# Optimization experiments

Hardware: AMD Instinct MI355X
Metric: run time of the kernel (lower is better)

The kernel has to match this reference:

```python
import jax, jax.numpy as jnp
import numpy as np

EPS = 1e-6
TTT_BASE_LR = 1.0
NUM_HEADS = 16


def _ln_fused_l2_bwd(x, l2_target, gamma, beta, eps=EPS):
    # Gradient of ||LN(x)*gamma+beta - target||^2/2 wrt x (fused LN + L2 bwd).
    mu = x.mean(axis=-1, keepdims=True)
    var = ((x - mu) ** 2).mean(axis=-1, keepdims=True)
    std = jnp.sqrt(var + eps)
    x_hat = (x - mu) / std
    grad_x_hat = (gamma * x_hat + beta - l2_target) * gamma
    z = (grad_x_hat
         - grad_x_hat.mean(axis=-1, keepdims=True)
         - x_hat * (grad_x_hat * x_hat).mean(axis=-1, keepdims=True)) / std
    return z


def _ln_fwd(x, gamma, beta, eps=EPS):
    mu = x.mean(axis=-1, keepdims=True)
    var = ((x - mu) ** 2).mean(axis=-1, keepdims=True)
    x_hat = (x - mu) / jnp.sqrt(var + eps)
    return gamma * x_hat + beta


def setup_inputs() -> dict:
    key = jax.random.key(0)
    ks = jax.random.split(key, 6)
    B, L, C, H = 2, 2048, 1024, NUM_HEADS
    D = C // H
    return {
        "hidden_states": jax.random.normal(ks[0], (B, L, C), jnp.float32),
        "Wq": jax.random.normal(ks[1], (C, C), jnp.float32) * 0.02,
        "Wk": jax.random.normal(ks[2], (C, C), jnp.float32) * 0.02,
        "Wv": jax.random.normal(ks[3], (C, C), jnp.float32) * 0.02,
        "W1": jax.random.normal(ks[4], (H, D, D), jnp.float32) * 0.02,
        "b1": jnp.zeros((H, 1, D), jnp.float32),
        "ttt_norm_weight": jnp.ones((H, D), jnp.float32),
        "ttt_norm_bias": jnp.zeros((H, D), jnp.float32),
        "lr_weight": jax.random.normal(ks[5], (H, C, 1), jnp.float32) * 0.02,
        "lr_bias": jnp.zeros((H, 1), jnp.float32),
    }


def reference(hidden_states, Wq, Wk, Wv, W1, b1,
              ttt_norm_weight, ttt_norm_bias, lr_weight, lr_bias):
    B, L, C = hidden_states.shape
    H = NUM_HEADS
    D = C // H

    def proj(W):  # nn.Linear(no bias): x @ W^T, then split heads -> [B,H,L,D]
        return (hidden_states @ W.T).reshape(B, L, H, D).transpose(0, 2, 1, 3)

    XQ, XK, XV = proj(Wq), proj(Wk), proj(Wv)

    # adaptive per-token learning rate eta: [B,H,L,1]
    ttt_lr = jnp.einsum("blc,hci->bhli", hidden_states, lr_weight)
    ttt_lr = jax.nn.sigmoid(ttt_lr + lr_bias.reshape(1, H, 1, 1))
    eta = TTT_BASE_LR * ttt_lr / D

    # inner-loop forward with initial fast weights W1,b1
    Z1 = jnp.einsum("bhld,hdf->bhlf", XK, W1) + b1[None]  # [B,H,L,D]
    recon_target = XV - XK

    gamma = ttt_norm_weight.reshape(1, H, 1, D)
    beta = ttt_norm_bias.reshape(1, H, 1, D)
    grad_l_wrt_Z1 = _ln_fused_l2_bwd(Z1, recon_target, gamma, beta)

    # dual form update (batch-parallel, no state carry)
    eg = eta * grad_l_wrt_Z1                               # [B,H,L,D]
    Attn1 = jnp.einsum("bhld,bhmd->bhlm", XQ, XK)          # [B,H,L,L]
    b1_bar = b1[None] - eg.sum(axis=2, keepdims=True)      # [B,H,1,D]
    Z1_bar = (jnp.einsum("bhld,hdf->bhlf", XQ, W1)
              - jnp.einsum("bhlm,bhmd->bhld", Attn1, eg)
              + b1_bar)

    Z1_normalized = _ln_fwd(Z1_bar, gamma, beta)
    return XQ + Z1_normalized  # [B,H,L,D]
```

## Files before the change

kernel.cpp:

```cpp
#include <hip/hip_runtime.h>
#include <math.h>

#define B_ 2
#define L_ 2048
#define C_ 1024
#define H_ 16
#define D_ 64
#define BH_ (B_*H_)
#define M_ (B_*L_)
#define N_ (3*C_)
#define K_ C_
#define EPS_ 1e-6f
#define NCHUNK_ 16
#define LDT_ 136
#define WTS_ 72

typedef unsigned short ushort_t;
typedef short short8 __attribute__((ext_vector_type(8)));
typedef float f32x4 __attribute__((ext_vector_type(4)));
typedef unsigned short ushort4_t __attribute__((ext_vector_type(4)));

__device__ __forceinline__ ushort_t f2bf(float f) {
    union { float f; unsigned u; } v; v.f = f;
    unsigned r = v.u + 0x7FFFu + ((v.u >> 16) & 1u);
    return (ushort_t)(r >> 16);
}
__device__ __forceinline__ float bf2f(ushort_t h) {
    union { unsigned u; float f; } v; v.u = ((unsigned)h) << 16;
    return v.f;
}

__device__ __forceinline__ void gload16(const void* g, void* l) {
    __builtin_amdgcn_global_load_lds(
        (const __attribute__((address_space(1))) void*)g,
        (__attribute__((address_space(3))) void*)l, 16, 0, 0);
}

__global__ __launch_bounds__(256) void cast_eta(
    const float* __restrict__ hs, const float* __restrict__ Wq,
    const float* __restrict__ Wk, const float* __restrict__ Wv,
    const float* __restrict__ W1, const float* __restrict__ lrw,
    const float* __restrict__ lrb, ushort_t* __restrict__ hsB,
    ushort_t* __restrict__ Wcat, float* __restrict__ eta,
    ushort_t* __restrict__ W1tg, float* __restrict__ W1tf) {
    __shared__ float pA[16][257], pB[16][257];
    const int bid = blockIdx.x, t = threadIdx.x;
    if (bid < 2048) {
        const int iA = bid * 2, iB = iA + 1;
        const float* rA = hs + (size_t)iA * C_;
        const float* rB = hs + (size_t)iB * C_;
        f32x4 a = *(const f32x4*)(rA + t * 4);
        f32x4 b = *(const f32x4*)(rB + t * 4);
        ushort4_t oa, ob;
        oa.x = f2bf(a.x); oa.y = f2bf(a.y); oa.z = f2bf(a.z); oa.w = f2bf(a.w);
        ob.x = f2bf(b.x); ob.y = f2bf(b.y); ob.z = f2bf(b.z); ob.w = f2bf(b.w);
        *(ushort4_t*)(hsB + (size_t)iA * C_ + t * 4) = oa;
        *(ushort4_t*)(hsB + (size_t)iB * C_ + t * 4) = ob;
        #pragma unroll
        for (int h = 0; h < 16; ++h) {
            f32x4 w = *(const f32x4*)(lrw + (size_t)h * C_ + t * 4);
            pA[h][t] = a.x * w.x + a.y * w.y + a.z * w.z + a.w * w.w;
            pB[h][t] = b.x * w.x + b.y * w.y + b.z * w.z + b.w * w.w;
        }
        __syncthreads();
        const int h = t >> 4, seg = t & 15;
        float sA = 0.f, sB = 0.f;
        #pragma unroll
        for (int j = 0; j < 16; ++j) {
            sA += pA[h][seg * 16 + j];
            sB += pB[h][seg * 16 + j];
        }
        #pragma unroll
        for (int m = 1; m < 16; m <<= 1) {
            sA += __shfl_xor(sA, m, 64);
            sB += __shfl_xor(sB, m, 64);
        }
        if (seg == 0) {
            float bb = lrb[h];
            int bA = iA >> 11, lA = iA & (L_ - 1);
            int bB = iB >> 11, lB = iB & (L_ - 1);
            eta[((size_t)(bA * H_ + h)) * L_ + lA] =
                (1.f / (1.f + expf(-(sA + bb)))) * (1.0f / 64.0f);
            eta[((size_t)(bB * H_ + h)) * L_ + lB] =
                (1.f / (1.f + expf(-(sB + bb)))) * (1.0f / 64.0f);
        }
    } else if (bid < 2816) {
        const int wb = bid - 2048;
        #pragma unroll
        for (int ii = 0; ii < 4; ++ii) {
            int cid = wb * 1024 + ii * 256 + t;
            int m = cid >> 18, r = cid & ((1 << 18) - 1);
            f32x4 v;
            if (m == 0)      v = *(const f32x4*)(Wq + (size_t)r * 4);
            else if (m == 1) v = *(const f32x4*)(Wk + (size_t)r * 4);
            else {
                f32x4 vv = *(const f32x4*)(Wv + (size_t)r * 4);
                f32x4 vk = *(const f32x4*)(Wk + (size_t)r * 4);
                v.x = vv.x - vk.x; v.y = vv.y - vk.y;
                v.z = vv.z - vk.z; v.w = vv.w - vk.w;
            }
            ushort4_t o;
            o.x = f2bf(v.x); o.y = f2bf(v.y); o.z = f2bf(v.z); o.w = f2bf(v.w);
            *(ushort4_t*)(Wcat + (size_t)m * (C_ * C_) + (size_t)r * 4) = o;
        }
    } else {
        const int h = bid - 2816;
        __shared__ float Wl[64 * 65];
        #pragma unroll
        for (int p = 0; p < 4; ++p) {
            int i4 = p * 256 + t;
            int e = i4 >> 4, f0 = (i4 & 15) * 4;
            f32x4 v = *(const f32x4*)(W1 + (size_t)h * 4096 + e * 64 + f0);
            Wl[(f0 + 0) * 65 + e] = v.x;
            Wl[(f0 + 1) * 65 + e] = v.y;
            Wl[(f0 + 2) * 65 + e] = v.z;
            Wl[(f0 + 3) * 65 + e] = v.w;
        }
        __syncthreads();
        #pragma unroll
        for (int p = 0; p < 16; ++p) {
            int flat = p * 256 + t;
            float v = Wl[(flat >> 6) * 65 + (flat & 63)];
            W1tf[(size_t)h * 4096 + flat] = v;
            W1tg[(size_t)h * 4096 + flat] = f2bf(v);
        }
    }
}

__global__ __launch_bounds__(256) void gemm_qkv(
    const ushort_t* __restrict__ A, const ushort_t* __restrict__ Bc,
    ushort_t* __restrict__ XQ, ushort_t* __restrict__ XK,
    ushort_t* __restrict__ XT) {
    __shared__ __align__(16) ushort_t smem[128 * 136];
    ushort_t* Al0 = smem;
    ushort_t* Bl0 = smem + 4096;
    ushort_t* Al1 = smem + 8192;
    ushort_t* Bl1 = smem + 12288;
    const int bm = blockIdx.x, bn = blockIdx.y;
    const int t = threadIdx.x, w = t >> 6, lane = t & 63;
    const int wr = w >> 1, wc = w & 1;
    const int la15 = lane & 15, la4 = lane >> 4;
    f32x4 acc[4][4];
    #pragma unroll
    for (int a = 0; a < 4; a++)
        #pragma unroll
        for (int b = 0; b < 4; b++)
            #pragma unroll
            for (int j = 0; j < 4; j++) acc[a][b][j] = 0.f;

    const int ci0 = w * 64 + lane;
    const int xread = (la15 >> 1) & 3;
    const int uslot = la4 ^ xread;
    const int r0 = ci0 >> 2,         kcp0 = (ci0 & 3) ^ ((r0 >> 1) & 3);
    const int r1 = (256 + ci0) >> 2, kcp1 = (ci0 & 3) ^ ((r1 >> 1) & 3);
    const ushort_t* gA0 = A + (size_t)(bm * 128 + r0) * K_ + kcp0 * 8;
    const ushort_t* gA1 = A + (size_t)(bm * 128 + r1) * K_ + kcp1 * 8;
    const ushort_t* gB0 = Bc + (size_t)(bn * 128 + r0) * K_ + kcp0 * 8;
    const ushort_t* gB1 = Bc + (size_t)(bn * 128 + r1) * K_ + kcp1 * 8;

#define COMPUTE_T(AL, BL) do {                                              \
        short8 af[4], bfv[4];                                               \
        _Pragma("unroll")                                                   \
        for (int mf = 0; mf < 4; ++mf)                                      \
            af[mf] = *(const short8*)&(AL)[(wr * 64 + mf * 16 + la15) * 32 + uslot * 8]; \
        _Pragma("unroll")                                                   \
        for (int nf = 0; nf < 4; ++nf)                                      \
            bfv[nf] = *(const short8*)&(BL)[(wc * 64 + nf * 16 + la15) * 32 + uslot * 8]; \
        _Pragma("unroll")                                                   \
        for (int mf = 0; mf < 4; ++mf)                                      \
            _Pragma("unroll")                                               \
            for (int nf = 0; nf < 4; ++nf)                                  \
                acc[mf][nf] = __builtin_amdgcn_mfma_f32_16x16x32_bf16(      \
                    af[mf], bfv[nf], acc[mf][nf], 0, 0, 0);                 \
    } while (0)

    for (int kt2 = 0; kt2 < 16; ++kt2) {
        const int kA = kt2 * 64, kB = kA + 32;
        __syncthreads();
        gload16(gA0 + kA, &Al0[w * 512]);
        gload16(gB0 + kA, &Bl0[w * 512]);
        gload16(gA1 + kA, &Al0[2048 + w * 512]);
        gload16(gB1 + kA, &Bl0[2048 + w * 512]);
        gload16(gA0 + kB, &Al1[w * 512]);
        gload16(gB0 + kB, &Bl1[w * 512]);
        gload16(gA1 + kB, &Al1[2048 + w * 512]);
        gload16(gB1 + kB, &Bl1[2048 + w * 512]);
        __syncthreads();
        COMPUTE_T(Al0, Bl0);
        COMPUTE_T(Al1, Bl1);
    }
#undef COMPUTE_T

    __syncthreads();
    #pragma unroll
    for (int mf = 0; mf < 4; ++mf)
        #pragma unroll
        for (int nf = 0; nf < 4; ++nf)
            #pragma unroll
            for (int rg = 0; rg < 4; ++rg) {
                int i = wr * 64 + mf * 16 + la4 * 4 + rg;
                int j = wc * 64 + nf * 16 + la15;
                smem[i * 136 + j] = f2bf(acc[mf][nf][rg]);
            }
    __syncthreads();
    const int jbase = bn * 128;
    const int mtx = jbase >> 10;
    ushort_t* dst = (mtx == 0) ? XQ : (mtx == 1 ? XK : XT);
    const int hb = (jbase & 1023) >> 6;
    #pragma unroll
    for (int pass = 0; pass < 8; ++pass) {
        int i = pass * 16 + (t >> 4);
        int jj = (t & 15) * 8;
        short8 v = *(const short8*)&smem[i * 136 + jj];
        int ig = bm * 128 + i;
        int b = ig >> 11, l = ig & (L_ - 1);
        int h = hb + (jj >> 6), d = jj & 63;
        *(short8*)&dst[((size_t)(b * H_ + h) * L_ + l) * D_ + d] = v;
    }
}

__global__ __launch_bounds__(256) void k2_grad2(
    const ushort_t* __restrict__ XK, const ushort_t* __restrict__ XT,
    const ushort_t* __restrict__ W1tg, const float* __restrict__ b1,
    const float* __restrict__ tw, const float* __restrict__ tb,
    const float* __restrict__ eta, float* __restrict__ GpT,
    float* __restrict__ bsump) {
    __shared__ __align__(16) ushort_t xkt[64 * LDT_];
    __shared__ __align__(16) ushort_t egl[64 * LDT_];
    __shared__ float b1s[64], gs[64], bes[64];
    __shared__ float sred[4][64];
    const int bh = blockIdx.y, lt = blockIdx.x;
    const int h = bh & (H_ - 1);
    const int t = threadIdx.x, w = t >> 6, lane = t & 63;
    const int la15 = lane & 15, la4 = lane >> 4;
    if (t < 64) { b1s[t] = b1[h * 64 + t]; gs[t] = tw[h * 64 + t]; bes[t] = tb[h * 64 + t]; }
    __syncthreads();

    const ushort_t* xk = XK + (size_t)bh * L_ * D_;
    const ushort_t* xt = XT + (size_t)bh * L_ * D_;
    const ushort_t* w1g = W1tg + (size_t)h * 4096;
    const int l0 = lt * 128 + w * 32;
    const int llw = w * 32;

    f32x4 acc[2][4];
    #pragma unroll
    for (int mf = 0; mf < 2; mf++)
        #pragma unroll
        for (int nf = 0; nf < 4; nf++) {
            float bv = b1s[nf * 16 + la15];
            #pragma unroll
            for (int j = 0; j < 4; j++) acc[mf][nf][j] = bv;
        }
    #pragma unroll
    for (int ks = 0; ks < 2; ++ks) {
        short8 af[2], bfv[4];
        const int d0 = ks * 32 + la4 * 8;
        #pragma unroll
        for (int mf = 0; mf < 2; mf++) {
            af[mf] = *(const short8*)&xk[(size_t)(l0 + mf * 16 + la15) * D_ + d0];
            const int ll = llw + mf * 16 + la15;
            #pragma unroll
            for (int jj = 0; jj < 8; jj++)
                xkt[(d0 + jj) * LDT_ + ll] = (ushort_t)af[mf][jj];
        }
        #pragma unroll
        for (int nf = 0; nf < 4; nf++)
            bfv[nf] = *(const short8*)&w1g[(nf * 16 + la15) * 64 + d0];
        #pragma unroll
        for (int mf = 0; mf < 2; mf++)
            #pragma unroll
            for (int nf = 0; nf < 4; nf++)
                acc[mf][nf] = __builtin_amdgcn_mfma_f32_16x16x32_bf16(
                    af[mf], bfv[nf], acc[mf][nf], 0, 0, 0);
    }

    const float* etap = eta + (size_t)bh * L_;
    float accbs[4] = {0.f, 0.f, 0.f, 0.f};
    #pragma unroll
    for (int mf = 0; mf < 2; ++mf) {
        #pragma unroll
        for (int rg = 0; rg < 4; ++rg) {
            int lrow = l0 + mf * 16 + (la4 << 2) + rg;
            int llr  = llw + mf * 16 + (la4 << 2) + rg;
            float x[4], xh[4], gh[4];
            #pragma unroll
            for (int nf = 0; nf < 4; nf++) x[nf] = acc[mf][nf][rg];
            float s = x[0] + x[1] + x[2] + x[3];
            float q = x[0]*x[0] + x[1]*x[1] + x[2]*x[2] + x[3]*x[3];
            s += __shfl_xor(s, 1, 64); q += __shfl_xor(q, 1, 64);
            s += __shfl_xor(s, 2, 64); q += __shfl_xor(q, 2, 64);
            s += __shfl_xor(s, 4, 64); q += __shfl_xor(q, 4, 64);
            s += __shfl_xor(s, 8, 64); q += __shfl_xor(q, 8, 64);
            float mu = s * (1.f / 64.f);
            float var = q * (1.f / 64.f) - mu * mu;
            float inv = 1.f / sqrtf(var + EPS_);
            float s1 = 0.f, s2 = 0.f;
            #pragma unroll
            for (int nf = 0; nf < 4; nf++) {
                int d = nf * 16 + la15;
                xh[nf] = (x[nf] - mu) * inv;
                float tgt = bf2f(xt[(size_t)lrow * D_ + d]);
                float g = gs[d];
                gh[nf] = (g * xh[nf] + bes[d] - tgt) * g;
                s1 += gh[nf]; s2 += gh[nf] * xh[nf];
            }
            s1 += __shfl_xor(s1, 1, 64); s2 += __shfl_xor(s2, 1, 64);
            s1 += __shfl_xor(s1, 2, 64); s2 += __shfl_xor(s2, 2, 64);
            s1 += __shfl_xor(s1, 4, 64); s2 += __shfl_xor(s2, 4, 64);
            s1 += __shfl_xor(s1, 8, 64); s2 += __shfl_xor(s2, 8, 64);
            float m1 = s1 * (1.f / 64.f), m2 = s2 * (1.f / 64.f);
            float el = etap[lrow];
            #pragma unroll
            for (int nf = 0; nf < 4; nf++) {
                int d = nf * 16 + la15;
                float egv = el * ((gh[nf] - m1 - xh[nf] * m2) * inv);
                accbs[nf] += egv;
                egl[d * LDT_ + llr] = f2bf(egv);
            }
        }
    }
    #pragma unroll
    for (int nf = 0; nf < 4; nf++) {
        accbs[nf] += __shfl_xor(accbs[nf], 16, 64);
        accbs[nf] += __shfl_xor(accbs[nf], 32, 64);
    }
    if (lane < 16)
        #pragma unroll
        for (int nf = 0; nf < 4; nf++) sred[w][nf * 16 + lane] = accbs[nf];
    __syncthreads();

    f32x4 aG[4];
    #pragma unroll
    for (int nf = 0; nf < 4; nf++)
        #pragma unroll
        for (int j = 0; j < 4; j++) aG[nf][j] = 0.f;
    #pragma unroll
    for (int ks = 0; ks < 4; ++ks) {
        const int ko = ks * 32 + la4 * 8;
        short8 ae = *(const short8*)&egl[(w * 16 + la15) * LDT_ + ko];
        #pragma unroll
        for (int nf = 0; nf < 4; nf++) {
            short8 be = *(const short8*)&xkt[(nf * 16 + la15) * LDT_ + ko];
            aG[nf] = __builtin_amdgcn_mfma_f32_16x16x32_bf16(ae, be, aG[nf], 0, 0, 0);
        }
    }
    float* gp = GpT + (size_t)(bh * NCHUNK_ + lt) * 4096;
    #pragma unroll
    for (int nf = 0; nf < 4; nf++)
        #pragma unroll
        for (int rg = 0; rg < 4; rg++) {
            int f = w * 16 + (la4 << 2) + rg;
            int e = nf * 16 + la15;
            gp[f * 64 + e] = aG[nf][rg];
        }
    if (t < 64)
        bsump[(bh * NCHUNK_ + lt) * 64 + t] =
            sred[0][t] + sred[1][t] + sred[2][t] + sred[3][t];
}

__global__ __launch_bounds__(256) void k2b_reduce(
    const float* __restrict__ GpT, const float* __restrict__ bsump,
    float* __restrict__ G, float* __restrict__ bsum) {
    const int seg = blockIdx.x, bh = blockIdx.y;
    const int t = threadIdx.x;
    #pragma unroll 2
    for (int ii = 0; ii < 2; ++ii) {
        int i = seg * 512 + ii * 256 + t;
        float s = 0.f;
        #pragma unroll
        for (int c = 0; c < NCHUNK_; c++)
            s += GpT[(size_t)(bh * NCHUNK_ + c) * 4096 + i];
        G[(size_t)bh * 4096 + i] = s;
    }
    if (seg == 0 && t < 64) {
        float s = 0.f;
        #pragma unroll
        for (int c = 0; c < NCHUNK_; c++)
            s += bsump[(bh * NCHUNK_ + c) * 64 + t];
        bsum[bh * 64 + t] = s;
    }
}

__global__ __launch_bounds__(256) void k3_out(
    const ushort_t* __restrict__ XQ, const float* __restrict__ W1tf,
    const float* __restrict__ G, const float* __restrict__ b1,
    const float* __restrict__ bsum, const float* __restrict__ tw,
    const float* __restrict__ tb, float* __restrict__ out) {
    __shared__ __align__(16) ushort_t Wt[64 * WTS_];
    __shared__ float b1s[64], gs[64], bes[64];
    const int bh = blockIdx.y, lt = blockIdx.x;
    const int h = bh & (H_ - 1);
    const int t = threadIdx.x, w = t >> 6, lane = t & 63;
    const int la15 = lane & 15, la4 = lane >> 4;
    for (int p = t; p < 4096; p += 256) {
        float s = W1tf[(size_t)h * 4096 + p] - G[(size_t)bh * 4096 + p];
        Wt[(p >> 6) * WTS_ + (p & 63)] = f2bf(s);
    }
    if (t < 64) {
        b1s[t] = b1[h * 64 + t] - bsum[bh * 64 + t];
        gs[t] = tw[h * 64 + t]; bes[t] = tb[h * 64 + t];
    }
    __syncthreads();

    const ushort_t* xq = XQ + (size_t)bh * L_ * D_;
    const int l0 = lt * 128 + w * 32;
    f32x4 acc[2][4];
    #pragma unroll
    for (int mf = 0; mf < 2; mf++)
        #pragma unroll
        for (int nf = 0; nf < 4; nf++) {
            float bv = b1s[nf * 16 + la15];
            #pragma unroll
            for (int j = 0; j < 4; j++) acc[mf][nf][j] = bv;
        }
    #pragma unroll
    for (int ks = 0; ks < 2; ++ks) {
        short8 af[2], bfv[4];
        const int d0 = ks * 32 + la4 * 8;
        #pragma unroll
        for (int mf = 0; mf < 2; mf++)
            af[mf] = *(const short8*)&xq[(size_t)(l0 + mf * 16 + la15) * D_ + d0];
        #pragma unroll
        for (int nf = 0; nf < 4; nf++)
            bfv[nf] = *(const short8*)&Wt[(nf * 16 + la15) * WTS_ + d0];
        #pragma unroll
        for (int mf = 0; mf < 2; mf++)
            #pragma unroll
            for (int nf = 0; nf < 4; nf++)
                acc[mf][nf] = __builtin_amdgcn_mfma_f32_16x16x32_bf16(
                    af[mf], bfv[nf], acc[mf][nf], 0, 0, 0);
    }

    float* outp = out + (size_t)bh * L_ * D_;
    #pragma unroll
    for (int mf = 0; mf < 2; ++mf) {
        #pragma unroll
        for (int rg = 0; rg < 4; ++rg) {
            int lrow = l0 + mf * 16 + (la4 << 2) + rg;
            float x[4];
            #pragma unroll
            for (int nf = 0; nf < 4; nf++) x[nf] = acc[mf][nf][rg];
            float s = x[0] + x[1] + x[2] + x[3];
            float q = x[0]*x[0] + x[1]*x[1] + x[2]*x[2] + x[3]*x[3];
            s += __shfl_xor(s, 1, 64); q += __shfl_xor(q, 1, 64);
            s += __shfl_xor(s, 2, 64); q += __shfl_xor(q, 2, 64);
            s += __shfl_xor(s, 4, 64); q += __shfl_xor(q, 4, 64);
            s += __shfl_xor(s, 8, 64); q += __shfl_xor(q, 8, 64);
            float mu = s * (1.f / 64.f);
            float var = q * (1.f / 64.f) - mu * mu;
            float inv = 1.f / sqrtf(var + EPS_);
            #pragma unroll
            for (int nf = 0; nf < 4; nf++) {
                int d = nf * 16 + la15;
                float xh = (x[nf] - mu) * inv;
                float o = gs[d] * xh + bes[d];
                float qv = bf2f(xq[(size_t)lrow * D_ + d]);
                outp[(size_t)lrow * D_ + d] = qv + o;
            }
        }
    }
}

extern "C" void kernel_launch(void* const* d_in, const int* in_sizes, int n_in,
                              void* d_out, int out_size, void* d_ws, size_t ws_size,
                              hipStream_t stream) {
    const float* hs  = (const float*)d_in[0];
    const float* Wq  = (const float*)d_in[1];
    const float* Wk  = (const float*)d_in[2];
    const float* Wv  = (const float*)d_in[3];
    const float* W1  = (const float*)d_in[4];
    const float* b1  = (const float*)d_in[5];
    const float* tw  = (const float*)d_in[6];
    const float* tb  = (const float*)d_in[7];
    const float* lrw = (const float*)d_in[8];
    const float* lrb = (const float*)d_in[9];
    float* out = (float*)d_out;

    char* ws = (char*)d_ws;
    size_t off = 0;
    ushort_t* hsB  = (ushort_t*)(ws + off); off += (size_t)M_ * K_ * 2;
    ushort_t* Wcat = (ushort_t*)(ws + off); off += (size_t)N_ * K_ * 2;
    ushort_t* XQ   = (ushort_t*)(ws + off); off += (size_t)M_ * C_ * 2;
    ushort_t* XK   = (ushort_t*)(ws + off); off += (size_t)M_ * C_ * 2;
    ushort_t* XT   = (ushort_t*)(ws + off); off += (size_t)M_ * C_ * 2;
    float*    eta  = (float*)(ws + off);    off += (size_t)BH_ * L_ * 4;
    ushort_t* W1tg = (ushort_t*)(ws + off); off += (size_t)H_ * D_ * D_ * 2;
    float*    W1tf = (float*)(ws + off);    off += (size_t)H_ * D_ * D_ * 4;
    float*    G    = (float*)(ws + off);    off += (size_t)BH_ * D_ * D_ * 4;
    float*    bsum = (float*)(ws + off);    off += (size_t)BH_ * D_ * 4;
    float*    GpT   = (float*)hsB;
    float*    bsump = (float*)Wcat;

    cast_eta<<<2048 + 768 + 16, 256, 0, stream>>>(hs, Wq, Wk, Wv, W1, lrw, lrb,
                                                  hsB, Wcat, eta, W1tg, W1tf);
    gemm_qkv<<<dim3(M_ / 128, N_ / 128), 256, 0, stream>>>(hsB, Wcat, XQ, XK, XT);
    k2_grad2<<<dim3(L_ / 128, BH_), 256, 0, stream>>>(XK, XT, W1tg, b1, tw, tb, eta, GpT, bsump);
    k2b_reduce<<<dim3(8, BH_), 256, 0, stream>>>(GpT, bsump, G, bsum);
    k3_out<<<dim3(L_ / 128, BH_), 256, 0, stream>>>(XQ, W1tf, G, b1, bsum, tw, tb, out);
}
```

Baseline: 78.94 us.

## Fold eta projection into QKV GEMM as an extra N tile

The per-head learning-rate projection (hidden_states · lr_weight) moves out of the cast kernel, which did it with fp32 dot products and a 32KB shared-memory reduction. Instead, lr_weight is cast to bf16 and appended to the concatenated weight matrix. The QKV GEMM gets one extra column tile whose epilogue applies the sigmoid and writes eta. This makes the cast kernel lighter and raises its occupancy, at the cost of a mostly-wasted 128-wide GEMM tile for 16 useful columns and bf16 precision for eta. The padding rows of the extra tile are left uninitialized, but only the first 16 columns are read.

Measured after the change: 85.96 us. 1.09x slower.

```diff
diff --git a/kernel.cpp b/kernel.cpp
--- a/kernel.cpp
+++ b/kernel.cpp
@@ -9,6 +9,7 @@
 #define BH_ (B_*H_)
 #define M_ (B_*L_)
 #define N_ (3*C_)
+#define NW_ 3200
 #define K_ C_
 #define EPS_ 1e-6f
 #define NCHUNK_ 16
@@ -36,55 +37,24 @@
         (__attribute__((address_space(3))) void*)l, 16, 0, 0);
 }
 
-__global__ __launch_bounds__(256) void cast_eta(
+__global__ __launch_bounds__(256) void cast_w(
     const float* __restrict__ hs, const float* __restrict__ Wq,
     const float* __restrict__ Wk, const float* __restrict__ Wv,
     const float* __restrict__ W1, const float* __restrict__ lrw,
-    const float* __restrict__ lrb, ushort_t* __restrict__ hsB,
-    ushort_t* __restrict__ Wcat, float* __restrict__ eta,
+    ushort_t* __restrict__ hsB, ushort_t* __restrict__ Wcat,
     ushort_t* __restrict__ W1tg, float* __restrict__ W1tf) {
-    __shared__ float pA[16][257], pB[16][257];
     const int bid = blockIdx.x, t = threadIdx.x;
     if (bid < 2048) {
-        const int iA = bid * 2, iB = iA + 1;
-        const float* rA = hs + (size_t)iA * C_;
-        const float* rB = hs + (size_t)iB * C_;
-        f32x4 a = *(const f32x4*)(rA + t * 4);
-        f32x4 b = *(const f32x4*)(rB + t * 4);
-        ushort4_t oa, ob;
-        oa.x = f2bf(a.x); oa.y = f2bf(a.y); oa.z = f2bf(a.z); oa.w = f2bf(a.w);
-        ob.x = f2bf(b.x); ob.y = f2bf(b.y); ob.z = f2bf(b.z); ob.w = f2bf(b.w);
-        *(ushort4_t*)(hsB + (size_t)iA * C_ + t * 4) = oa;
-        *(ushort4_t*)(hsB + (size_t)iB * C_ + t * 4) = ob;
-        #pragma unroll
-        for (int h = 0; h < 16; ++h) {
-            f32x4 w = *(const f32x4*)(lrw + (size_t)h * C_ + t * 4);
-            pA[h][t] = a.x * w.x + a.y * w.y + a.z * w.z + a.w * w.w;
-            pB[h][t] = b.x * w.x + b.y * w.y + b.z * w.z + b.w * w.w;
-        }
-        __syncthreads();
-        const int h = t >> 4, seg = t & 15;
-        float sA = 0.f, sB = 0.f;
-        #pragma unroll
-        for (int j = 0; j < 16; ++j) {
-            sA += pA[h][seg * 16 + j];
-            sB += pB[h][seg * 16 + j];
-        }
-        #pragma unroll
-        for (int m = 1; m < 16; m <<= 1) {
-            sA += __shfl_xor(sA, m, 64);
-            sB += __shfl_xor(sB, m, 64);
-        }
-        if (seg == 0) {
-            float bb = lrb[h];
-            int bA = iA >> 11, lA = iA & (L_ - 1);
-            int bB = iB >> 11, lB = iB & (L_ - 1);
-            eta[((size_t)(bA * H_ + h)) * L_ + lA] =
-                (1.f / (1.f + expf(-(sA + bb)))) * (1.0f / 64.0f);
-            eta[((size_t)(bB * H_ + h)) * L_ + lB] =
-                (1.f / (1.f + expf(-(sB + bb)))) * (1.0f / 64.0f);
-        }
-    } else if (bid < 2816) {
+        const int iA = bid * 2;
+        #pragma unroll
+        for (int rr = 0; rr < 2; ++rr) {
+            const float* r = hs + (size_t)(iA + rr) * C_;
+            f32x4 a = *(const f32x4*)(r + t * 4);
+            ushort4_t o;
+            o.x = f2bf(a.x); o.y = f2bf(a.y); o.z = f2bf(a.z); o.w = f2bf(a.w);
+            *(ushort4_t*)(hsB + (size_t)(iA + rr) * C_ + t * 4) = o;
+        }
+    } else if (bid < 2820) {
         const int wb = bid - 2048;
         #pragma unroll
         for (int ii = 0; ii < 4; ++ii) {
@@ -93,18 +63,20 @@
             f32x4 v;
             if (m == 0)      v = *(const f32x4*)(Wq + (size_t)r * 4);
             else if (m == 1) v = *(const f32x4*)(Wk + (size_t)r * 4);
-            else {
+            else if (m == 2) {
                 f32x4 vv = *(const f32x4*)(Wv + (size_t)r * 4);
                 f32x4 vk = *(const f32x4*)(Wk + (size_t)r * 4);
                 v.x = vv.x - vk.x; v.y = vv.y - vk.y;
                 v.z = vv.z - vk.z; v.w = vv.w - vk.w;
+            } else {
+                v = *(const f32x4*)(lrw + (size_t)r * 4);
             }
             ushort4_t o;
             o.x = f2bf(v.x); o.y = f2bf(v.y); o.z = f2bf(v.z); o.w = f2bf(v.w);
             *(ushort4_t*)(Wcat + (size_t)m * (C_ * C_) + (size_t)r * 4) = o;
         }
     } else {
-        const int h = bid - 2816;
+        const int h = bid - 2820;
         __shared__ float Wl[64 * 65];
         #pragma unroll
         for (int p = 0; p < 4; ++p) {
@@ -130,7 +102,8 @@
 __global__ __launch_bounds__(256) void gemm_qkv(
     const ushort_t* __restrict__ A, const ushort_t* __restrict__ Bc,
     ushort_t* __restrict__ XQ, ushort_t* __restrict__ XK,
-    ushort_t* __restrict__ XT) {
+    ushort_t* __restrict__ XT, const float* __restrict__ lrb,
+    float* __restrict__ eta) {
     __shared__ __align__(16) ushort_t smem[128 * 136];
     ushort_t* Al0 = smem;
     ushort_t* Bl0 = smem + 4096;
@@ -190,6 +163,23 @@
         COMPUTE_T(Al1, Bl1);
     }
 #undef COMPUTE_T
+
+    if (bn == 24) {
+        if (wc == 0) {
+            const float bb = lrb[la15];
+            #pragma unroll
+            for (int mf = 0; mf < 4; ++mf)
+                #pragma unroll
+                for (int rg = 0; rg < 4; ++rg) {
+                    int i = bm * 128 + wr * 64 + mf * 16 + la4 * 4 + rg;
+                    int b = i >> 11, l = i & (L_ - 1);
+                    float x = acc[mf][0][rg] + bb;
+                    eta[((size_t)(b * H_ + la15)) * L_ + l] =
+                        (1.f / (1.f + expf(-x))) * (1.0f / 64.0f);
+                }
+        }
+        return;
+    }
 
     __syncthreads();
     #pragma unroll
@@ -479,7 +469,7 @@
     char* ws = (char*)d_ws;
     size_t off = 0;
     ushort_t* hsB  = (ushort_t*)(ws + off); off += (size_t)M_ * K_ * 2;
-    ushort_t* Wcat = (ushort_t*)(ws + off); off += (size_t)N_ * K_ * 2;
+    ushort_t* Wcat = (ushort_t*)(ws + off); off += (size_t)NW_ * K_ * 2;
     ushort_t* XQ   = (ushort_t*)(ws + off); off += (size_t)M_ * C_ * 2;
     ushort_t* XK   = (ushort_t*)(ws + off); off += (size_t)M_ * C_ * 2;
     ushort_t* XT   = (ushort_t*)(ws + off); off += (size_t)M_ * C_ * 2;
@@ -491,9 +481,9 @@
     float*    GpT   = (float*)hsB;
     float*    bsump = (float*)Wcat;
 
-    cast_eta<<<2048 + 768 + 16, 256, 0, stream>>>(hs, Wq, Wk, Wv, W1, lrw, lrb,
-                                                  hsB, Wcat, eta, W1tg, W1tf);
-    gemm_qkv<<<dim3(M_ / 128, N_ / 128), 256, 0, stream>>>(hsB, Wcat, XQ, XK, XT);
+    cast_w<<<2048 + 772 + 16, 256, 0, stream>>>(hs, Wq, Wk, Wv, W1, lrw,
+                                                hsB, Wcat, W1tg, W1tf);
+    gemm_qkv<<<dim3(M_ / 128, 25), 256, 0, stream>>>(hsB, Wcat, XQ, XK, XT, lrb, eta);
     k2_grad2<<<dim3(L_ / 128, BH_), 256, 0, stream>>>(XK, XT, W1tg, b1, tw, tb, eta, GpT, bsump);
     k2b_reduce<<<dim3(8, BH_), 256, 0, stream>>>(GpT, bsump, G, bsum);
     k3_out<<<dim3(L_ / 128, BH_), 256, 0, stream>>>(XQ, W1tf, G, b1, bsum, tw, tb, out);
```

## Simplify QKV GEMM to single 32-wide K stage with direct global stores

Applied to the files above, without the earlier changes.

Reverts the QKV projection GEMM from a two-stage, 64-wide K step per barrier pair back to one 32-wide K step per iteration. LDS use drops from a 128x136 buffer to two 128x32 tiles. The epilogue now writes each accumulator element as a scalar bf16 global store instead of staging through LDS for coalesced 16-byte writes. This lowers LDS footprint and could raise occupancy, but it doubles the number of barrier pairs and makes the output stores uncoalesced 2-byte writes.

After: 78.21 us (median of 2 runs). About the same (-0.9%).

```diff
diff --git a/kernel.cpp b/kernel.cpp
--- a/kernel.cpp
+++ b/kernel.cpp
@@ -131,11 +131,8 @@
     const ushort_t* __restrict__ A, const ushort_t* __restrict__ Bc,
     ushort_t* __restrict__ XQ, ushort_t* __restrict__ XK,
     ushort_t* __restrict__ XT) {
-    __shared__ __align__(16) ushort_t smem[128 * 136];
-    ushort_t* Al0 = smem;
-    ushort_t* Bl0 = smem + 4096;
-    ushort_t* Al1 = smem + 8192;
-    ushort_t* Bl1 = smem + 12288;
+    __shared__ __align__(16) ushort_t Al[128 * 32];
+    __shared__ __align__(16) ushort_t Bl[128 * 32];
     const int bm = blockIdx.x, bn = blockIdx.y;
     const int t = threadIdx.x, w = t >> 6, lane = t & 63;
     const int wr = w >> 1, wc = w & 1;
@@ -151,72 +148,50 @@
     const int ci0 = w * 64 + lane;
     const int xread = (la15 >> 1) & 3;
     const int uslot = la4 ^ xread;
-    const int r0 = ci0 >> 2,         kcp0 = (ci0 & 3) ^ ((r0 >> 1) & 3);
-    const int r1 = (256 + ci0) >> 2, kcp1 = (ci0 & 3) ^ ((r1 >> 1) & 3);
-    const ushort_t* gA0 = A + (size_t)(bm * 128 + r0) * K_ + kcp0 * 8;
-    const ushort_t* gA1 = A + (size_t)(bm * 128 + r1) * K_ + kcp1 * 8;
-    const ushort_t* gB0 = Bc + (size_t)(bn * 128 + r0) * K_ + kcp0 * 8;
-    const ushort_t* gB1 = Bc + (size_t)(bn * 128 + r1) * K_ + kcp1 * 8;
-
-#define COMPUTE_T(AL, BL) do {                                              \
-        short8 af[4], bfv[4];                                               \
-        _Pragma("unroll")                                                   \
-        for (int mf = 0; mf < 4; ++mf)                                      \
-            af[mf] = *(const short8*)&(AL)[(wr * 64 + mf * 16 + la15) * 32 + uslot * 8]; \
-        _Pragma("unroll")                                                   \
-        for (int nf = 0; nf < 4; ++nf)                                      \
-            bfv[nf] = *(const short8*)&(BL)[(wc * 64 + nf * 16 + la15) * 32 + uslot * 8]; \
-        _Pragma("unroll")                                                   \
-        for (int mf = 0; mf < 4; ++mf)                                      \
-            _Pragma("unroll")                                               \
-            for (int nf = 0; nf < 4; ++nf)                                  \
-                acc[mf][nf] = __builtin_amdgcn_mfma_f32_16x16x32_bf16(      \
-                    af[mf], bfv[nf], acc[mf][nf], 0, 0, 0);                 \
-    } while (0)
-
-    for (int kt2 = 0; kt2 < 16; ++kt2) {
-        const int kA = kt2 * 64, kB = kA + 32;
+
+    for (int kt = 0; kt < K_ / 32; ++kt) {
         __syncthreads();
-        gload16(gA0 + kA, &Al0[w * 512]);
-        gload16(gB0 + kA, &Bl0[w * 512]);
-        gload16(gA1 + kA, &Al0[2048 + w * 512]);
-        gload16(gB1 + kA, &Bl0[2048 + w * 512]);
-        gload16(gA0 + kB, &Al1[w * 512]);
-        gload16(gB0 + kB, &Bl1[w * 512]);
-        gload16(gA1 + kB, &Al1[2048 + w * 512]);
-        gload16(gB1 + kB, &Bl1[2048 + w * 512]);
+        #pragma unroll
+        for (int q = 0; q < 2; ++q) {
+            int ci = q * 256 + ci0;
+            int r = ci >> 2, kc = ci & 3;
+            int kcp = kc ^ ((r >> 1) & 3);
+            gload16(A + (size_t)(bm * 128 + r) * K_ + kt * 32 + kcp * 8,
+                    &Al[q * 2048 + w * 512]);
+            gload16(Bc + (size_t)(bn * 128 + r) * K_ + kt * 32 + kcp * 8,
+                    &Bl[q * 2048 + w * 512]);
+        }
         __syncthreads();
-        COMPUTE_T(Al0, Bl0);
-        COMPUTE_T(Al1, Bl1);
-    }
-#undef COMPUTE_T
-
-    __syncthreads();
-    #pragma unroll
-    for (int mf = 0; mf < 4; ++mf)
+        short8 af[4], bfv[4];
+        #pragma unroll
+        for (int mf = 0; mf < 4; ++mf)
+            af[mf] = *(const short8*)&Al[(wr * 64 + mf * 16 + la15) * 32 + uslot * 8];
         #pragma unroll
         for (int nf = 0; nf < 4; ++nf)
-            #pragma unroll
-            for (int rg = 0; rg < 4; ++rg) {
-                int i = wr * 64 + mf * 16 + la4 * 4 + rg;
-                int j = wc * 64 + nf * 16 + la15;
-                smem[i * 136 + j] = f2bf(acc[mf][nf][rg]);
-            }
-    __syncthreads();
+            bfv[nf] = *(const short8*)&Bl[(wc * 64 + nf * 16 + la15) * 32 + uslot * 8];
+        #pragma unroll
+        for (int mf = 0; mf < 4; ++mf)
+            #pragma unroll
+            for (int nf = 0; nf < 4; ++nf)
+                acc[mf][nf] = __builtin_amdgcn_mfma_f32_16x16x32_bf16(
+                    af[mf], bfv[nf], acc[mf][nf], 0, 0, 0);
+    }
+
     const int jbase = bn * 128;
     const int mtx = jbase >> 10;
     ushort_t* dst = (mtx == 0) ? XQ : (mtx == 1 ? XK : XT);
-    const int hb = (jbase & 1023) >> 6;
-    #pragma unroll
-    for (int pass = 0; pass < 8; ++pass) {
-        int i = pass * 16 + (t >> 4);
-        int jj = (t & 15) * 8;
-        short8 v = *(const short8*)&smem[i * 136 + jj];
-        int ig = bm * 128 + i;
-        int b = ig >> 11, l = ig & (L_ - 1);
-        int h = hb + (jj >> 6), d = jj & 63;
-        *(short8*)&dst[((size_t)(b * H_ + h) * L_ + l) * D_ + d] = v;
-    }
+    #pragma unroll
+    for (int mf = 0; mf < 4; ++mf)
+        #pragma unroll
+        for (int nf = 0; nf < 4; ++nf)
+            #pragma unroll
+            for (int rg = 0; rg < 4; ++rg) {
+                int i = bm * 128 + wr * 64 + mf * 16 + (la4 << 2) + rg;
+                int j = (jbase & 1023) + wc * 64 + nf * 16 + la15;
+                int b = i >> 11, l = i & (L_ - 1);
+                int h = j >> 6, d = j & 63;
+                dst[((size_t)(b * H_ + h) * L_ + l) * D_ + d] = f2bf(acc[mf][nf][rg]);
+            }
 }
 
 __global__ __launch_bounds__(256) void k2_grad2(
```
